# Performance work log

Measured on AMD Instinct MI355X. Metric: run time of the kernel, lower is better.

The kernel has to match this reference:

```python
import jax, jax.numpy as jnp
import numpy as np

D = 1024      # n_embd
H = 16        # n_head
HD = D // H   # head_size = 64


def _layernorm(x, g, b, eps=1e-5):
    mu = jnp.mean(x, axis=-1, keepdims=True)
    var = jnp.mean((x - mu) ** 2, axis=-1, keepdims=True)
    return (x - mu) * jax.lax.rsqrt(var + eps) * g + b


def setup_inputs() -> dict:
    key = jax.random.key(0)
    ks = jax.random.split(key, 12)
    s = lambda fan_in: 1.0 / np.sqrt(fan_in)
    inp = {
        "x": jax.random.normal(ks[0], (4, 2048, D), dtype=jnp.float32),
        # attention projections (bias=False in Head), per-head weights fused into [D, D]
        "wq": jax.random.uniform(ks[1], (D, D), jnp.float32, -s(D), s(D)),
        "wk": jax.random.uniform(ks[2], (D, D), jnp.float32, -s(D), s(D)),
        "wv": jax.random.uniform(ks[3], (D, D), jnp.float32, -s(D), s(D)),
        "wo": jax.random.uniform(ks[4], (D, D), jnp.float32, -s(D), s(D)),
        "bo": jax.random.uniform(ks[5], (D,), jnp.float32, -s(D), s(D)),
        # feed-forward: D -> 4D -> D
        "w1": jax.random.uniform(ks[6], (D, 4 * D), jnp.float32, -s(D), s(D)),
        "b1": jax.random.uniform(ks[7], (4 * D,), jnp.float32, -s(D), s(D)),
        "w2": jax.random.uniform(ks[8], (4 * D, D), jnp.float32, -s(4 * D), s(4 * D)),
        "b2": jax.random.uniform(ks[9], (D,), jnp.float32, -s(4 * D), s(4 * D)),
        # layernorms
        "g_ln1": jnp.ones((D,), jnp.float32),
        "b_ln1": jnp.zeros((D,), jnp.float32),
        "g_ln2": jnp.ones((D,), jnp.float32),
        "b_ln2": jnp.zeros((D,), jnp.float32),
    }
    return inp


def reference(x, wq, wk, wv, wo, bo, w1, b1, w2, b2, g_ln1, b_ln1, g_ln2, b_ln2):
    B, T, _ = x.shape
    # --- self-attention on ln1(x) ---
    h = _layernorm(x, g_ln1, b_ln1)
    q = (h @ wq).reshape(B, T, H, HD)
    k = (h @ wk).reshape(B, T, H, HD)
    v = (h @ wv).reshape(B, T, H, HD)
    scores = jnp.einsum("bqhd,bkhd->bhqk", q, k) * (HD ** -0.5)
    causal = jnp.tril(jnp.ones((T, T), dtype=bool))
    scores = jnp.where(causal, scores, -jnp.inf)
    wei = jax.nn.softmax(scores, axis=-1)                    # [B,H,T,T]
    attn = jnp.einsum("bhqk,bkhd->bqhd", wei, v).reshape(B, T, D)
    x = x + attn @ wo + bo
    # --- feed-forward on ln2(x) ---
    h2 = _layernorm(x, g_ln2, b_ln2)
    x = x + jax.nn.relu(h2 @ w1 + b1) @ w2 + b2
    return x
```

## Files before the change

kernel.cpp:

```cpp
#include <hip/hip_runtime.h>
#include <cstdint>

typedef __bf16 bf16x8 __attribute__((ext_vector_type(8)));
typedef float f32x4 __attribute__((ext_vector_type(4)));
typedef unsigned int u32x4 __attribute__((ext_vector_type(4)));
typedef unsigned int u32x2 __attribute__((ext_vector_type(2)));
typedef unsigned short u16x4 __attribute__((ext_vector_type(4)));

#define D_MODEL 1024
#define SEQ     2048
#define NBATCH  4
#define NHEAD   16
#define HDIM    64
#define NTOK    (NBATCH * SEQ)
#define QSCALE  0.18033688011112042f

__device__ __forceinline__ unsigned short f2bf(float f) {
  unsigned int u = __builtin_bit_cast(unsigned int, f);
  u += 0x7FFFu + ((u >> 16) & 1u);
  return (unsigned short)(u >> 16);
}

__device__ __forceinline__ float bf2f(unsigned short s) {
  return __builtin_bit_cast(float, (unsigned int)s << 16);
}

__device__ __forceinline__ bf16x8 load8bf(const unsigned short* p) {
  return __builtin_bit_cast(bf16x8, *(const u32x4*)p);
}

__device__ __forceinline__ f32x4 mfma16(bf16x8 a, bf16x8 b, f32x4 c) {
  return __builtin_amdgcn_mfma_f32_16x16x32_bf16(a, b, c, 0, 0, 0);
}

__device__ __forceinline__ void gload16(const unsigned short* g, unsigned short* l) {
  __builtin_amdgcn_global_load_lds((__attribute__((address_space(1))) void*)g,
                                   (__attribute__((address_space(3))) void*)l, 16, 0, 0);
}

__global__ __launch_bounds__(256) void tcast_all(const float* __restrict__ wq,
                                                 const float* __restrict__ wk,
                                                 const float* __restrict__ wv,
                                                 const float* __restrict__ wo,
                                                 const float* __restrict__ w1,
                                                 const float* __restrict__ w2,
                                                 unsigned short* __restrict__ wqkv_t,
                                                 unsigned short* __restrict__ wo_t,
                                                 unsigned short* __restrict__ w1_t,
                                                 unsigned short* __restrict__ w2_t) {
  const int id = blockIdx.x;
  const float* in; unsigned short* out; int K, N, k0, n0;
  if (id < 4096) {
    const int seg = id >> 10, r = id & 1023;
    in  = seg == 0 ? wq : seg == 1 ? wk : seg == 2 ? wv : wo;
    out = seg == 3 ? wo_t : wqkv_t + (size_t)seg * 1024 * 1024;
    K = 1024; N = 1024; n0 = (r & 31) * 32; k0 = (r >> 5) * 32;
  } else if (id < 8192) {
    const int r = id - 4096;
    in = w1; out = w1_t; K = 1024; N = 4096;
    n0 = (r & 127) * 32; k0 = (r >> 7) * 32;
  } else {
    const int r = id - 8192;
    in = w2; out = w2_t; K = 4096; N = 1024;
    n0 = (r & 31) * 32; k0 = (r >> 5) * 32;
  }
  __shared__ float tile[32][33];
  const int tx = threadIdx.x & 31, ty = threadIdx.x >> 5;
  #pragma unroll
  for (int j = 0; j < 4; ++j)
    tile[ty + 8 * j][tx] = in[(size_t)(k0 + ty + 8 * j) * N + n0 + tx];
  __syncthreads();
  #pragma unroll
  for (int j = 0; j < 4; ++j)
    out[(size_t)(n0 + ty + 8 * j) * K + k0 + tx] = f2bf(tile[tx][ty + 8 * j]);
}

template <int FPIN>
__global__ __launch_bounds__(256) void ln_kernel(const void* __restrict__ xin,
                                                 const float* __restrict__ g,
                                                 const float* __restrict__ bb,
                                                 unsigned short* __restrict__ out) {
  const int row = blockIdx.x, tid = threadIdx.x;
  float4 xv;
  if (FPIN) {
    xv = ((const float4*)((const float*)xin + (size_t)row * D_MODEL))[tid];
  } else {
    const u16x4 bv4 = ((const u16x4*)((const unsigned short*)xin + (size_t)row * D_MODEL))[tid];
    xv.x = bf2f(bv4.x); xv.y = bf2f(bv4.y); xv.z = bf2f(bv4.z); xv.w = bf2f(bv4.w);
  }
  float s  = xv.x + xv.y + xv.z + xv.w;
  float ss = xv.x * xv.x + xv.y * xv.y + xv.z * xv.z + xv.w * xv.w;
  #pragma unroll
  for (int off = 1; off < 64; off <<= 1) { s += __shfl_xor(s, off); ss += __shfl_xor(ss, off); }
  __shared__ float red[8];
  const int wave = tid >> 6, lane = tid & 63;
  if (lane == 0) { red[wave] = s; red[4 + wave] = ss; }
  __syncthreads();
  s  = red[0] + red[1] + red[2] + red[3];
  ss = red[4] + red[5] + red[6] + red[7];
  const float mu   = s * (1.0f / D_MODEL);
  const float var  = ss * (1.0f / D_MODEL) - mu * mu;
  const float rstd = rsqrtf(var + 1e-5f);
  const float4 gv = ((const float4*)g)[tid];
  const float4 bv = ((const float4*)bb)[tid];
  u16x4 o;
  o.x = f2bf((xv.x - mu) * rstd * gv.x + bv.x);
  o.y = f2bf((xv.y - mu) * rstd * gv.y + bv.y);
  o.z = f2bf((xv.z - mu) * rstd * gv.z + bv.z);
  o.w = f2bf((xv.w - mu) * rstd * gv.w + bv.w);
  *(u16x4*)(out + (size_t)row * D_MODEL + tid * 4) = o;
}

template <bool BIAS, bool RELU, int RES, bool OBF, bool QKV>
__global__ __launch_bounds__(256) void gemm_bt(const unsigned short* __restrict__ A,
                                               const unsigned short* __restrict__ Bt,
                                               const float* __restrict__ bias,
                                               const void* __restrict__ res,
                                               void* __restrict__ out,
                                               unsigned short* __restrict__ qb,
                                               unsigned short* __restrict__ kp,
                                               unsigned short* __restrict__ vt,
                                               int M, int N, int K) {
  __shared__ __align__(16) unsigned short As[128 * 64];
  __shared__ __align__(16) unsigned short Bs[128 * 64];
  const int tid  = threadIdx.x;
  const int lin = blockIdx.y * gridDim.x + blockIdx.x;
  const int xcd = lin & 7, idx = lin >> 3;
  const int by = xcd * 8 + (idx & 7);
  const int bx = idx >> 3;
  const int row0 = by * 128, col0 = bx * 128;
  const int wave = tid >> 6, lane = tid & 63;
  const int wm = wave >> 1, wn = wave & 1;
  const int l15 = lane & 15, quad = lane >> 4;
  f32x4 acc[4][4] = {};

  const int tr = tid >> 3;
  const int tc = (tid & 7) ^ (tr & 7);
  const unsigned short* gA = A  + (size_t)(row0 + tr) * K + tc * 8;
  const unsigned short* gB = Bt + (size_t)(col0 + tr) * K + tc * 8;

  const int rowA = (wm * 64 + l15) * 64;
  const int rowB = (wn * 64 + l15) * 64;
  const int swz0 = (quad ^ (l15 & 7)) * 8;
  const int swz1 = ((4 + quad) ^ (l15 & 7)) * 8;

  for (int k0 = 0; k0 < K; k0 += 64) {
    #pragma unroll
    for (int i = 0; i < 4; ++i) {
      gload16(gA + (size_t)(i * 32) * K + k0, As + (i * 256 + tid) * 8);
      gload16(gB + (size_t)(i * 32) * K + k0, Bs + (i * 256 + tid) * 8);
    }
    __syncthreads();
    #pragma unroll
    for (int kf = 0; kf < 2; ++kf) {
      const int swz = kf ? swz1 : swz0;
      bf16x8 af[4], bfr[4];
      #pragma unroll
      for (int t = 0; t < 4; ++t) {
        af[t]  = load8bf(As + rowA + t * 1024 + swz);
        bfr[t] = load8bf(Bs + rowB + t * 1024 + swz);
      }
      #pragma unroll
      for (int i = 0; i < 4; ++i)
        #pragma unroll
        for (int j = 0; j < 4; ++j)
          acc[i][j] = mfma16(af[i], bfr[j], acc[i][j]);
    }
    __syncthreads();
  }

  const size_t rbase = (size_t)row0 + wm * 64 + quad * 4;
  const int cbase = col0 + wn * 64 + l15;
  if (QKV) {
    const int sec = col0 >> 10;
    #pragma unroll
    for (int i = 0; i < 4; ++i) {
      #pragma unroll
      for (int j = 0; j < 4; ++j) {
        const int col = cbase + j * 16;
        if (sec == 0) {
          #pragma unroll
          for (int r = 0; r < 4; ++r) {
            const size_t row = rbase + i * 16 + r;
            qb[row * 1024 + col] = f2bf(acc[i][j][r] * QSCALE);
          }
        } else if (sec == 1) {
          const int c2 = col - 1024, hh = c2 >> 6, d = c2 & 63;
          #pragma unroll
          for (int r = 0; r < 4; ++r) {
            const size_t row = rbase + i * 16 + r;
            const int bb = (int)(row >> 11), t = (int)(row & 2047);
            kp[(((size_t)(bb * 16 + hh)) * SEQ + t) * 64 + d] = f2bf(acc[i][j][r]);
          }
        } else {
          const int c2 = col - 2048, hh = c2 >> 6, d = c2 & 63;
          const size_t t0 = rbase + i * 16;
          const int bb = (int)(t0 >> 11);
          u16x4 pk;
          #pragma unroll
          for (int r = 0; r < 4; ++r) pk[r] = f2bf(acc[i][j][r]);
          *(u16x4*)(vt + ((size_t)(bb * 16 + hh) * 64 + d) * SEQ + (t0 & 2047)) = pk;
        }
      }
    }
  } else {
    #pragma unroll
    for (int i = 0; i < 4; ++i) {
      #pragma unroll
      for (int j = 0; j < 4; ++j) {
        const int col = cbase + j * 16;
        const float bval = BIAS ? bias[col] : 0.0f;
        #pragma unroll
        for (int r = 0; r < 4; ++r) {
          const size_t row = rbase + i * 16 + r;
          float v = acc[i][j][r];
          if (BIAS) v += bval;
          if (RELU) v = fmaxf(v, 0.0f);
          if (RES == 1) v += ((const float*)res)[row * N + col];
          if (RES == 2) v += bf2f(((const unsigned short*)res)[row * N + col]);
          if (OBF)  ((unsigned short*)out)[row * N + col] = f2bf(v);
          else      ((float*)out)[row * N + col] = v;
        }
      }
    }
  }
}

__global__ __launch_bounds__(256) void attn5(const unsigned short* __restrict__ qb,
                                             const unsigned short* __restrict__ kp,
                                             const unsigned short* __restrict__ vt,
                                             unsigned short* __restrict__ attnb) {
  const int lin = (blockIdx.z * 16 + blockIdx.y) * 8 + blockIdx.x;
  const int xcd = lin & 7, idx = lin >> 3;
  const int bh = xcd * 8 + (idx >> 3);
  const int xb = idx & 7;
  const int b = bh >> 4, h = bh & 15;
  const int tid = threadIdx.x, wave = tid >> 6, lane = tid & 63;
  const int l15 = lane & 15, quad = lane >> 4;
  const size_t tokbase = (size_t)b * SEQ;

  __shared__ __align__(16) unsigned short ks[64 * 64];
  __shared__ __align__(16) unsigned short vts[64 * 64];
  __shared__ __align__(16) unsigned short plds[4][32 * 64];

  const unsigned short* kbase = kp + (size_t)bh * SEQ * HDIM;
  const unsigned short* vbase = vt + (size_t)bh * HDIM * SEQ;

  for (int half = 0; half < 2; ++half) {
    const int qblk = (half == 0) ? (15 - xb) : xb;
    const int qw0 = qblk * 128 + wave * 32;

    bf16x8 qf[2][2];
    #pragma unroll
    for (int qfi = 0; qfi < 2; ++qfi)
      #pragma unroll
      for (int kf = 0; kf < 2; ++kf)
        qf[qfi][kf] = load8bf(qb + (tokbase + qw0 + qfi * 16 + l15) * 1024
                              + h * HDIM + kf * 32 + quad * 8);

    f32x4 o[2][4] = {};
    float lsum[2] = {0.0f, 0.0f};

    const int ntiles = qblk * 2 + 2;
    for (int kt = 0; kt < ntiles; ++kt) {
      const int k0 = kt * 64;
      __syncthreads();
      #pragma unroll
      for (int i = 0; i < 2; ++i) {
        const int cid = i * 256 + tid;
        const int r = cid >> 3, p = cid & 7, c = p ^ (r & 7);
        gload16(kbase + (size_t)(k0 + r) * HDIM + c * 8, ks + cid * 8);
      }
      #pragma unroll
      for (int i = 0; i < 2; ++i) {
        const int cid = i * 256 + tid;
        const int d = cid >> 3, p = cid & 7, c = p ^ (d & 7);
        gload16(vbase + (size_t)d * SEQ + k0 + c * 8, vts + cid * 8);
      }
      __syncthreads();
      if (k0 <= qw0 + 31) {
        f32x4 s[4][2] = {};
        #pragma unroll
        for (int kf = 0; kf < 2; ++kf)
          #pragma unroll
          for (int keyf = 0; keyf < 4; ++keyf) {
            const int row = keyf * 16 + l15;
            const int p = (kf * 4 + quad) ^ (row & 7);
            const bf16x8 kfr = load8bf(ks + row * 64 + p * 8);
            s[keyf][0] = mfma16(kfr, qf[0][kf], s[keyf][0]);
            s[keyf][1] = mfma16(kfr, qf[1][kf], s[keyf][1]);
          }
        #pragma unroll
        for (int qfi = 0; qfi < 2; ++qfi) {
          const int q = qw0 + qfi * 16 + l15;
          const int qloc = qfi * 16 + l15;
          #pragma unroll
          for (int keyf = 0; keyf < 4; ++keyf) {
            unsigned int pw[4];
            #pragma unroll
            for (int r = 0; r < 4; ++r) {
              const int key = k0 + keyf * 16 + quad * 4 + r;
              float p = __builtin_amdgcn_exp2f(s[keyf][qfi][r]);
              p = (key > q) ? 0.0f : p;
              pw[r] = __builtin_bit_cast(unsigned int, p);
              lsum[qfi] += __builtin_bit_cast(float, pw[r] & 0xFFFF0000u);
            }
            u32x2 packed;
            packed.x = (pw[0] >> 16) | (pw[1] & 0xFFFF0000u);
            packed.y = (pw[2] >> 16) | (pw[3] & 0xFFFF0000u);
            const int slot = (keyf * 4 + quad) ^ ((l15 & 7) << 1);
            *(u32x2*)(&plds[wave][qloc * 64 + slot * 4]) = packed;
          }
        }
        __builtin_amdgcn_s_waitcnt(0);
        #pragma unroll
        for (int kf = 0; kf < 2; ++kf) {
          bf16x8 pa[2];
          #pragma unroll
          for (int mf = 0; mf < 2; ++mf) {
            const int lq = mf * 16 + l15;
            const int c = (kf * 4 + quad) ^ (l15 & 7);
            pa[mf] = load8bf(&plds[wave][lq * 64 + c * 8]);
          }
          #pragma unroll
          for (int df = 0; df < 4; ++df) {
            const int row = df * 16 + l15;
            const int p = (kf * 4 + quad) ^ (row & 7);
            const bf16x8 vb = load8bf(vts + row * 64 + p * 8);
            o[0][df] = mfma16(pa[0], vb, o[0][df]);
            o[1][df] = mfma16(pa[1], vb, o[1][df]);
          }
        }
      }
    }
    #pragma unroll
    for (int mf = 0; mf < 2; ++mf) {
      float l = lsum[mf];
      l += __shfl_xor(l, 16);
      l += __shfl_xor(l, 32);
      const float rl = 1.0f / l;
      #pragma unroll
      for (int r = 0; r < 4; ++r) {
        const float rv = __shfl(rl, quad * 4 + r);
        const size_t row = tokbase + qw0 + mf * 16 + quad * 4 + r;
        #pragma unroll
        for (int df = 0; df < 4; ++df)
          attnb[row * D_MODEL + h * HDIM + df * 16 + l15] = f2bf(o[mf][df][r] * rv);
      }
    }
  }
}

extern "C" void kernel_launch(void* const* d_in, const int* in_sizes, int n_in,
                              void* d_out, int out_size, void* d_ws, size_t ws_size,
                              hipStream_t stream) {
  const float* x    = (const float*)d_in[0];
  const float* wq   = (const float*)d_in[1];
  const float* wk   = (const float*)d_in[2];
  const float* wv   = (const float*)d_in[3];
  const float* wo   = (const float*)d_in[4];
  const float* bo   = (const float*)d_in[5];
  const float* w1   = (const float*)d_in[6];
  const float* b1   = (const float*)d_in[7];
  const float* w2   = (const float*)d_in[8];
  const float* b2   = (const float*)d_in[9];
  const float* g1   = (const float*)d_in[10];
  const float* bl1  = (const float*)d_in[11];
  const float* g2   = (const float*)d_in[12];
  const float* bl2  = (const float*)d_in[13];
  float* out = (float*)d_out;

  char* ws = (char*)d_ws;
  size_t off = 0;
  auto alloc = [&](size_t bytes) { char* p = ws + off; off += (bytes + 255) & ~(size_t)255; return p; };
  unsigned short* wqkv_t = (unsigned short*)alloc((size_t)3072 * 1024 * 2);
  unsigned short* wo_t   = (unsigned short*)alloc((size_t)1024 * 1024 * 2);
  unsigned short* w1_t   = (unsigned short*)alloc((size_t)4096 * 1024 * 2);
  unsigned short* w2_t   = (unsigned short*)alloc((size_t)1024 * 4096 * 2);
  unsigned short* h1     = (unsigned short*)alloc((size_t)NTOK * 1024 * 2);
  unsigned short* kpb    = (unsigned short*)alloc((size_t)NTOK * 1024 * 2);
  unsigned short* vtb    = (unsigned short*)alloc((size_t)NTOK * 1024 * 2);
  unsigned short* attnb  = (unsigned short*)alloc((size_t)NTOK * 1024 * 2);
  unsigned short* h2     = (unsigned short*)alloc((size_t)NTOK * 1024 * 2);
  unsigned short* ffn1   = (unsigned short*)alloc((size_t)NTOK * 4096 * 2);
  unsigned short* qb  = attnb;
  unsigned short* x1b = h1;

  tcast_all<<<12288, 256, 0, stream>>>(wq, wk, wv, wo, w1, w2,
                                       wqkv_t, wo_t, w1_t, w2_t);
  ln_kernel<1><<<NTOK, 256, 0, stream>>>(x, g1, bl1, h1);
  gemm_bt<false, false, 0, true, true><<<dim3(24, 64), 256, 0, stream>>>(
      h1, wqkv_t, nullptr, nullptr, nullptr, qb, kpb, vtb, NTOK, 3072, 1024);
  attn5<<<dim3(SEQ / 256, NHEAD, NBATCH), 256, 0, stream>>>(qb, kpb, vtb, attnb);
  gemm_bt<true, false, 1, true, false><<<dim3(8, 64), 256, 0, stream>>>(
      attnb, wo_t, bo, x, x1b, nullptr, nullptr, nullptr, NTOK, 1024, 1024);
  ln_kernel<0><<<NTOK, 256, 0, stream>>>(x1b, g2, bl2, h2);
  gemm_bt<true, true, 0, true, false><<<dim3(32, 64), 256, 0, stream>>>(
      h2, w1_t, b1, nullptr, ffn1, nullptr, nullptr, nullptr, NTOK, 4096, 1024);
  gemm_bt<true, false, 2, false, false><<<dim3(8, 64), 256, 0, stream>>>(
      ffn1, w2_t, b2, x1b, out, nullptr, nullptr, nullptr, NTOK, 1024, 4096);
  (void)in_sizes; (void)n_in; (void)out_size; (void)ws_size;
}
```

Baseline: 471.6 us.

## Add 256x256-tile 512-thread GEMM with interleaved staging for QKV and FFN

```diff
diff --git a/kernel.cpp b/kernel.cpp
--- a/kernel.cpp
+++ b/kernel.cpp
@@ -226,6 +226,204 @@
   }
 }
 
+__device__ __forceinline__ void stage_half_512(const unsigned short* __restrict__ src,
+                                               unsigned short* dst, int K, int k0,
+                                               int h, int tid) {
+  #pragma unroll
+  for (int l = 0; l < 2; ++l) {
+    const int cid = l * 512 + tid;
+    const int r = cid >> 3, p = cid & 7, c = p ^ (r & 7);
+    gload16(src + (size_t)(h * 128 + r) * K + k0 + c * 8, dst + h * 8192 + cid * 8);
+  }
+}
+
+template <bool BIAS, bool RELU, int RES, bool OBF, bool QKV>
+__global__ __launch_bounds__(512, 2) void gemm256(const unsigned short* __restrict__ A,
+                                                  const unsigned short* __restrict__ Bt,
+                                                  const float* __restrict__ bias,
+                                                  const void* __restrict__ res,
+                                                  void* __restrict__ out,
+                                                  unsigned short* __restrict__ qb,
+                                                  unsigned short* __restrict__ kp,
+                                                  unsigned short* __restrict__ vt,
+                                                  int M, int N, int K) {
+  __shared__ __align__(16) unsigned short lds[2][32768];
+  const int tid = threadIdx.x;
+  const int lin = blockIdx.y * gridDim.x + blockIdx.x;
+  const int xcd = lin & 7, idx = lin >> 3;
+  const int by = xcd * 4 + (idx & 3);
+  const int bx = idx >> 2;
+  const int row0 = by * 256, col0 = bx * 256;
+  const int wave = tid >> 6, lane = tid & 63;
+  const int wm = wave >> 2, wn = wave & 3;
+  const int l15 = lane & 15, quad = lane >> 4;
+  const int swz0 = (quad ^ (l15 & 7)) * 8;
+  const int swz1 = ((4 + quad) ^ (l15 & 7)) * 8;
+
+  const unsigned short* gA = A  + (size_t)row0 * K;
+  const unsigned short* gB = Bt + (size_t)col0 * K;
+
+  unsigned short* As0 = &lds[0][0];
+  unsigned short* Bs0 = &lds[0][16384];
+  unsigned short* As1 = &lds[1][0];
+  unsigned short* Bs1 = &lds[1][16384];
+
+  f32x4 acc[8][4] = {};
+  const int KT = K >> 6;
+
+  stage_half_512(gA, As0, K, 0, 0, tid);
+  stage_half_512(gA, As0, K, 0, 1, tid);
+  stage_half_512(gB, Bs0, K, 0, 0, tid);
+  stage_half_512(gB, Bs0, K, 0, 1, tid);
+  stage_half_512(gB, Bs1, K, 64, 0, tid);
+  stage_half_512(gB, Bs1, K, 64, 1, tid);
+  asm volatile("s_waitcnt vmcnt(4)" ::: "memory");
+  asm volatile("s_barrier" ::: "memory");
+
+  for (int t = 0; t < KT; ++t) {
+    unsigned short* As  = (t & 1) ? As1 : As0;
+    unsigned short* Bs  = (t & 1) ? Bs1 : Bs0;
+    unsigned short* Asn = (t & 1) ? As0 : As1;
+    const int k1 = (t + 1) << 6, k2 = (t + 2) << 6;
+    bf16x8 a0[2][4], b01[2][2], b23[2][2];
+
+    #pragma unroll
+    for (int i = 0; i < 4; ++i) {
+      const unsigned short* ap = As + (wm * 128 + i * 16 + l15) * 64;
+      a0[0][i] = load8bf(ap + swz0);
+      a0[1][i] = load8bf(ap + swz1);
+    }
+    #pragma unroll
+    for (int j = 0; j < 2; ++j) {
+      const unsigned short* bp = Bs + (wn * 64 + j * 16 + l15) * 64;
+      b01[0][j] = load8bf(bp + swz0);
+      b01[1][j] = load8bf(bp + swz1);
+    }
+    if (t + 1 < KT) stage_half_512(gA, Asn, K, k1, 0, tid);
+    asm volatile("s_barrier" ::: "memory");
+    __builtin_amdgcn_s_setprio(1);
+    #pragma unroll
+    for (int kf = 0; kf < 2; ++kf)
+      #pragma unroll
+      for (int i = 0; i < 4; ++i)
+        #pragma unroll
+        for (int j = 0; j < 2; ++j)
+          acc[i][j] = mfma16(a0[kf][i], b01[kf][j], acc[i][j]);
+    __builtin_amdgcn_s_setprio(0);
+    asm volatile("s_barrier" ::: "memory");
+
+    #pragma unroll
+    for (int j = 0; j < 2; ++j) {
+      const unsigned short* bp = Bs + (wn * 64 + 32 + j * 16 + l15) * 64;
+      b23[0][j] = load8bf(bp + swz0);
+      b23[1][j] = load8bf(bp + swz1);
+    }
+    if (t + 1 < KT) stage_half_512(gA, Asn, K, k1, 1, tid);
+    asm volatile("s_barrier" ::: "memory");
+    __builtin_amdgcn_s_setprio(1);
+    #pragma unroll
+    for (int kf = 0; kf < 2; ++kf)
+      #pragma unroll
+      for (int i = 0; i < 4; ++i)
+        #pragma unroll
+        for (int j = 0; j < 2; ++j)
+          acc[i][2 + j] = mfma16(a0[kf][i], b23[kf][j], acc[i][2 + j]);
+    __builtin_amdgcn_s_setprio(0);
+    asm volatile("s_barrier" ::: "memory");
+
+    #pragma unroll
+    for (int i = 0; i < 4; ++i) {
+      const unsigned short* ap = As + (wm * 128 + 64 + i * 16 + l15) * 64;
+      a0[0][i] = load8bf(ap + swz0);
+      a0[1][i] = load8bf(ap + swz1);
+    }
+    if (t + 2 < KT) stage_half_512(gB, Bs, K, k2, 0, tid);
+    asm volatile("s_barrier" ::: "memory");
+    __builtin_amdgcn_s_setprio(1);
+    #pragma unroll
+    for (int kf = 0; kf < 2; ++kf)
+      #pragma unroll
+      for (int i = 0; i < 4; ++i)
+        #pragma unroll
+        for (int j = 0; j < 2; ++j)
+          acc[4 + i][2 + j] = mfma16(a0[kf][i], b23[kf][j], acc[4 + i][2 + j]);
+    __builtin_amdgcn_s_setprio(0);
+    asm volatile("s_barrier" ::: "memory");
+
+    if (t + 2 < KT) stage_half_512(gB, Bs, K, k2, 1, tid);
+    asm volatile("s_barrier" ::: "memory");
+    __builtin_amdgcn_s_setprio(1);
+    #pragma unroll
+    for (int kf = 0; kf < 2; ++kf)
+      #pragma unroll
+      for (int i = 0; i < 4; ++i)
+        #pragma unroll
+        for (int j = 0; j < 2; ++j)
+          acc[4 + i][j] = mfma16(a0[kf][i], b01[kf][j], acc[4 + i][j]);
+    __builtin_amdgcn_s_setprio(0);
+    if (t + 2 < KT) asm volatile("s_waitcnt vmcnt(4)" ::: "memory");
+    else            asm volatile("s_waitcnt vmcnt(0)" ::: "memory");
+    asm volatile("s_barrier" ::: "memory");
+  }
+
+  const size_t rbase = (size_t)row0 + wm * 128 + quad * 4;
+  const int cbase = col0 + wn * 64 + l15;
+  if (QKV) {
+    const int sec = col0 >> 10;
+    #pragma unroll
+    for (int i = 0; i < 8; ++i) {
+      #pragma unroll
+      for (int j = 0; j < 4; ++j) {
+        const int col = cbase + j * 16;
+        if (sec == 0) {
+          #pragma unroll
+          for (int r = 0; r < 4; ++r) {
+            const size_t row = rbase + i * 16 + r;
+            qb[row * 1024 + col] = f2bf(acc[i][j][r] * QSCALE);
+          }
+        } else if (sec == 1) {
+          const int c2 = col - 1024, hh = c2 >> 6, d = c2 & 63;
+          #pragma unroll
+          for (int r = 0; r < 4; ++r) {
+            const size_t row = rbase + i * 16 + r;
+            const int bb = (int)(row >> 11), tt = (int)(row & 2047);
+            kp[(((size_t)(bb * 16 + hh)) * SEQ + tt) * 64 + d] = f2bf(acc[i][j][r]);
+          }
+        } else {
+          const int c2 = col - 2048, hh = c2 >> 6, d = c2 & 63;
+          const size_t t0 = rbase + i * 16;
+          const int bb = (int)(t0 >> 11);
+          u16x4 pk;
+          #pragma unroll
+          for (int r = 0; r < 4; ++r) pk[r] = f2bf(acc[i][j][r]);
+          *(u16x4*)(vt + ((size_t)(bb * 16 + hh) * 64 + d) * SEQ + (t0 & 2047)) = pk;
+        }
+      }
+    }
+  } else {
+    #pragma unroll
+    for (int i = 0; i < 8; ++i) {
+      #pragma unroll
+      for (int j = 0; j < 4; ++j) {
+        const int col = cbase + j * 16;
+        const float bval = BIAS ? bias[col] : 0.0f;
+        #pragma unroll
+        for (int r = 0; r < 4; ++r) {
+          const size_t row = rbase + i * 16 + r;
+          float v = acc[i][j][r];
+          if (BIAS) v += bval;
+          if (RELU) v = fmaxf(v, 0.0f);
+          if (RES == 1) v += ((const float*)res)[row * N + col];
+          if (RES == 2) v += bf2f(((const unsigned short*)res)[row * N + col]);
+          if (OBF)  ((unsigned short*)out)[row * N + col] = f2bf(v);
+          else      ((float*)out)[row * N + col] = v;
+        }
+      }
+    }
+  }
+  (void)M;
+}
+
 __global__ __launch_bounds__(256) void attn5(const unsigned short* __restrict__ qb,
                                              const unsigned short* __restrict__ kp,
                                              const unsigned short* __restrict__ vt,
@@ -389,15 +587,15 @@
   tcast_all<<<12288, 256, 0, stream>>>(wq, wk, wv, wo, w1, w2,
                                        wqkv_t, wo_t, w1_t, w2_t);
   ln_kernel<1><<<NTOK, 256, 0, stream>>>(x, g1, bl1, h1);
-  gemm_bt<false, false, 0, true, true><<<dim3(24, 64), 256, 0, stream>>>(
+  gemm256<false, false, 0, true, true><<<dim3(12, 32), 512, 0, stream>>>(
       h1, wqkv_t, nullptr, nullptr, nullptr, qb, kpb, vtb, NTOK, 3072, 1024);
   attn5<<<dim3(SEQ / 256, NHEAD, NBATCH), 256, 0, stream>>>(qb, kpb, vtb, attnb);
   gemm_bt<true, false, 1, true, false><<<dim3(8, 64), 256, 0, stream>>>(
       attnb, wo_t, bo, x, x1b, nullptr, nullptr, nullptr, NTOK, 1024, 1024);
   ln_kernel<0><<<NTOK, 256, 0, stream>>>(x1b, g2, bl2, h2);
-  gemm_bt<true, true, 0, true, false><<<dim3(32, 64), 256, 0, stream>>>(
+  gemm256<true, true, 0, true, false><<<dim3(16, 32), 512, 0, stream>>>(
       h2, w1_t, b1, nullptr, ffn1, nullptr, nullptr, nullptr, NTOK, 4096, 1024);
-  gemm_bt<true, false, 2, false, false><<<dim3(8, 64), 256, 0, stream>>>(
+  gemm256<true, false, 2, false, false><<<dim3(4, 32), 512, 0, stream>>>(
       ffn1, w2_t, b2, x1b, out, nullptr, nullptr, nullptr, NTOK, 1024, 4096);
   (void)in_sizes; (void)n_in; (void)out_size; (void)ws_size;
 }
```

After: 503.8 us. +6.8%, slower.
